# Kernel tuning notes

Hardware: AMD Instinct MI355X
Metric: run time of the kernel (lower is better)

The kernel has to match this reference:

```python
import jax, jax.numpy as jnp
import numpy as np

V, D, G, E, B, S = 50000, 300, 256, 1600000, 64, 64


def setup_inputs() -> dict:
    key = jax.random.key(0)
    k = jax.random.split(key, 6)
    emb = jax.random.normal(k[0], (V, D), jnp.float32) * 0.02
    emb = emb.at[0].set(0.0)  # padding_idx=0
    W1 = jax.random.normal(k[1], (D, G), jnp.float32) * (1.0 / np.sqrt(D))
    b1 = jnp.zeros((G,), jnp.float32)
    W2 = jax.random.normal(k[2], (G, G), jnp.float32) * (1.0 / np.sqrt(G))
    b2 = jnp.zeros((G,), jnp.float32)
    edge_index = jax.random.randint(k[3], (2, E), 0, V, dtype=jnp.int64)
    word_ids = jax.random.randint(k[4], (B, S), 0, V, dtype=jnp.int64)
    return {"emb": emb, "W1": W1, "b1": b1, "W2": W2, "b2": b2,
            "edge_index": edge_index, "word_ids": word_ids}


def _gcn_conv(x, W, b, src, dst, num_nodes):
    """PyG GCNConv: add self-loops, symmetric deg^{-1/2} normalization.
    out_i = sum_{j->i} h_j / sqrt(deg_j * deg_i) + h_i / deg_i + b,
    with deg_i = 1 (self-loop) + in-degree(i), h = x @ W."""
    h = x @ W                                        # (N, G)
    deg = jnp.ones((num_nodes,), h.dtype).at[dst].add(1.0)
    inv_sqrt = jax.lax.rsqrt(deg)                    # (N,)
    coef = inv_sqrt[src] * inv_sqrt[dst]             # (E,)
    agg = jnp.zeros_like(h).at[dst].add(h[src] * coef[:, None])
    agg = agg + h * (inv_sqrt * inv_sqrt)[:, None]   # self-loop term
    return agg + b


def reference(emb, W1, b1, W2, b2, edge_index, word_ids):
    num_nodes = emb.shape[0]
    src, dst = edge_index[0], edge_index[1]
    h = jax.nn.relu(_gcn_conv(emb, W1, b1, src, dst, num_nodes))  # (V, G)
    h = _gcn_conv(h, W2, b2, src, dst, num_nodes)                 # (V, G)
    return h[word_ids]                                            # (B, S, G)
```

## Files before the change

### kernel.cpp

```cpp
#include <hip/hip_runtime.h>
#include <hip/hip_bf16.h>

#define NV 50000
#define ND 300
#define NDP 320
#define NG 256
#define NE 1600000
#define NBS 4096
#define NBUCK 196
#define EPB 8192
#define CPAD 16
#define GEMM1_BLOCKS 782

typedef short short8 __attribute__((ext_vector_type(8)));
typedef float f32x4 __attribute__((ext_vector_type(4)));
typedef float f32x2 __attribute__((ext_vector_type(2)));
typedef _Float16 half4 __attribute__((ext_vector_type(4)));

__device__ __forceinline__ ushort f2bf(float f) {
    unsigned u = __builtin_bit_cast(unsigned, f);
    unsigned r = (u + 0x7fffu + ((u >> 16) & 1u)) >> 16;
    return (ushort)r;
}
__device__ __forceinline__ float bf2f(ushort h) {
    unsigned u = ((unsigned)h) << 16;
    return __builtin_bit_cast(float, u);
}

__global__ __launch_bounds__(256) void hist_bucket(const int* __restrict__ dst,
                                                   int* __restrict__ bucket_count) {
    __shared__ int bh[NBUCK];
    int t = threadIdx.x;
    for (int b = t; b < NBUCK; b += 256) bh[b] = 0;
    __syncthreads();
    for (int i = blockIdx.x * 256 + t; i * 4 < NE; i += gridDim.x * 256) {
        int4 d = *(const int4*)(dst + i * 4);
        atomicAdd(&bh[d.x >> 8], 1);
        atomicAdd(&bh[d.y >> 8], 1);
        atomicAdd(&bh[d.z >> 8], 1);
        atomicAdd(&bh[d.w >> 8], 1);
    }
    __syncthreads();
    for (int b = t; b < NBUCK; b += 256)
        if (bh[b]) atomicAdd(&bucket_count[b * CPAD], bh[b]);
}

__global__ __launch_bounds__(256) void bucket_scan(const int* __restrict__ bucket_count,
                                                   int* __restrict__ bucket_base,
                                                   int* __restrict__ bucket_cursor) {
    __shared__ int s[256];
    int t = threadIdx.x;
    int v = (t < NBUCK) ? bucket_count[t * CPAD] : 0;
    s[t] = v;
    __syncthreads();
    for (int d = 1; d < 256; d <<= 1) {
        int x = (t >= d) ? s[t - d] : 0;
        __syncthreads();
        s[t] += x;
        __syncthreads();
    }
    int excl = s[t] - v;
    if (t < NBUCK) {
        bucket_base[t] = excl;
        bucket_cursor[t * CPAD] = excl;
    }
    if (t == 255) bucket_base[NBUCK] = s[255];
}

__global__ __launch_bounds__(256) void splitw_all(const float* __restrict__ W1,
                                                  const float* __restrict__ W2,
                                                  ushort* __restrict__ W1Th,
                                                  ushort* __restrict__ W1Tl,
                                                  ushort* __restrict__ W2Th,
                                                  ushort* __restrict__ W2Tl) {
    int idx = blockIdx.x * 256 + threadIdx.x;
    if (idx < NG * NDP) {
        int n = idx / NDP, k = idx - n * NDP;
        float v = (k < ND) ? W1[(size_t)k * NG + n] : 0.f;
        ushort h = f2bf(v);
        W1Th[idx] = h;
        W1Tl[idx] = f2bf(v - bf2f(h));
    } else {
        int j = idx - NG * NDP;
        if (j >= NG * NG) return;
        int n = j / NG, k = j - n * NG;
        float v = W2[(size_t)k * NG + n];
        ushort h = f2bf(v);
        W2Th[j] = h;
        W2Tl[j] = f2bf(v - bf2f(h));
    }
}

__global__ __launch_bounds__(256) void gemm1_scatter(const float* __restrict__ A,
                                                     const ushort* __restrict__ BTh,
                                                     const ushort* __restrict__ BTl,
                                                     unsigned char* __restrict__ C8,
                                                     const int* __restrict__ ei,
                                                     int* __restrict__ bucket_cursor,
                                                     unsigned* __restrict__ rec) {
    int t = threadIdx.x;
    if (blockIdx.x < GEMM1_BLOCKS) {
        __shared__ short Ah[128][40];
        __shared__ short Bh[128][40];
        __shared__ short Bl[128][40];
        const int lda = ND, ldb = NDP, M = NV, K = ND, KP = NDP;
        int bid = blockIdx.x;
        int bm = (bid % 391) * 128;
        int bn = (bid / 391) * 128;
        int lane = t & 63, wv = t >> 6;
        int wm = (wv >> 1) * 64, wn = (wv & 1) * 64;
        int srow = t >> 1;
        int skq = (t & 1) * 16;
        f32x4 acc[4][4];
#pragma unroll
        for (int mi = 0; mi < 4; ++mi)
#pragma unroll
            for (int ni = 0; ni < 4; ++ni) acc[mi][ni] = (f32x4)0.0f;

        for (int k0 = 0; k0 < KP; k0 += 32) {
            int gk = k0 + skq;
            {
                int gr = bm + srow;
                short va[16];
                float v[16];
                if (gr < M && gk < K) {
                    if (gk + 16 <= K) {
#pragma unroll
                        for (int q = 0; q < 4; ++q) {
                            float4 p = *(const float4*)(A + (size_t)gr * lda + gk + q * 4);
                            v[q * 4 + 0] = p.x; v[q * 4 + 1] = p.y;
                            v[q * 4 + 2] = p.z; v[q * 4 + 3] = p.w;
                        }
                    } else {
#pragma unroll
                        for (int e = 0; e < 16; ++e)
                            v[e] = (gk + e < K) ? A[(size_t)gr * lda + gk + e] : 0.f;
                    }
                } else {
#pragma unroll
                    for (int e = 0; e < 16; ++e) v[e] = 0.f;
                }
#pragma unroll
                for (int e = 0; e < 16; ++e) va[e] = (short)f2bf(v[e]);
                *(short8*)&Ah[srow][skq] = *(short8*)&va[0];
                *(short8*)&Ah[srow][skq + 8] = *(short8*)&va[8];
            }
            {
                int nr = bn + srow;
                short8 bh0 = *(const short8*)(BTh + (size_t)nr * ldb + gk);
                short8 bh1 = *(const short8*)(BTh + (size_t)nr * ldb + gk + 8);
                short8 bl0 = *(const short8*)(BTl + (size_t)nr * ldb + gk);
                short8 bl1 = *(const short8*)(BTl + (size_t)nr * ldb + gk + 8);
                *(short8*)&Bh[srow][skq] = bh0;
                *(short8*)&Bh[srow][skq + 8] = bh1;
                *(short8*)&Bl[srow][skq] = bl0;
                *(short8*)&Bl[srow][skq + 8] = bl1;
            }
            __syncthreads();
            int m16 = lane & 15, kb = (lane >> 4) * 8;
            short8 a_h[4], b_h[4], b_l[4];
#pragma unroll
            for (int mi = 0; mi < 4; ++mi)
                a_h[mi] = *(const short8*)&Ah[wm + mi * 16 + m16][kb];
#pragma unroll
            for (int ni = 0; ni < 4; ++ni) {
                b_h[ni] = *(const short8*)&Bh[wn + ni * 16 + m16][kb];
                b_l[ni] = *(const short8*)&Bl[wn + ni * 16 + m16][kb];
            }
#pragma unroll
            for (int mi = 0; mi < 4; ++mi)
#pragma unroll
                for (int ni = 0; ni < 4; ++ni) {
                    acc[mi][ni] = __builtin_amdgcn_mfma_f32_16x16x32_bf16(a_h[mi], b_h[ni], acc[mi][ni], 0, 0, 0);
                    acc[mi][ni] = __builtin_amdgcn_mfma_f32_16x16x32_bf16(a_h[mi], b_l[ni], acc[mi][ni], 0, 0, 0);
                }
            __syncthreads();
        }
        int m16 = lane & 15, rq = lane >> 4;
#pragma unroll
        for (int mi = 0; mi < 4; ++mi)
#pragma unroll
            for (int ni = 0; ni < 4; ++ni) {
                int row0 = bm + wm + mi * 16 + rq * 4;
                int col = bn + wn + ni * 16 + m16;
                int p01 = __builtin_amdgcn_cvt_pk_fp8_f32(acc[mi][ni][0], acc[mi][ni][1], 0, false);
                int p23 = __builtin_amdgcn_cvt_pk_fp8_f32(acc[mi][ni][2], acc[mi][ni][3], 0, false);
                if (row0 + 0 < M) C8[(size_t)(row0 + 0) * NG + col] = (unsigned char)(p01 & 0xff);
                if (row0 + 1 < M) C8[(size_t)(row0 + 1) * NG + col] = (unsigned char)((p01 >> 8) & 0xff);
                if (row0 + 2 < M) C8[(size_t)(row0 + 2) * NG + col] = (unsigned char)(p23 & 0xff);
                if (row0 + 3 < M) C8[(size_t)(row0 + 3) * NG + col] = (unsigned char)((p23 >> 8) & 0xff);
            }
    } else {
        __shared__ int cnt[NBUCK];
        __shared__ int basel[NBUCK];
        int e0 = (blockIdx.x - GEMM1_BLOCKS) * EPB;
        for (int b = t; b < NBUCK; b += 256) cnt[b] = 0;
        __syncthreads();
        for (int q = 0; q < EPB / 1024; ++q) {
            int i4 = e0 + q * 1024 + t * 4;
            if (i4 < NE) {
                int4 d = *(const int4*)(ei + NE + i4);
                atomicAdd(&cnt[d.x >> 8], 1);
                atomicAdd(&cnt[d.y >> 8], 1);
                atomicAdd(&cnt[d.z >> 8], 1);
                atomicAdd(&cnt[d.w >> 8], 1);
            }
        }
        __syncthreads();
        for (int b = t; b < NBUCK; b += 256) {
            int c = cnt[b];
            basel[b] = c ? atomicAdd(&bucket_cursor[b * CPAD], c) : 0;
        }
        __syncthreads();
        for (int b = t; b < NBUCK; b += 256) cnt[b] = 0;
        __syncthreads();
        for (int q = 0; q < EPB / 1024; ++q) {
            int i4 = e0 + q * 1024 + t * 4;
            if (i4 < NE) {
                int4 s = *(const int4*)(ei + i4);
                int4 d = *(const int4*)(ei + NE + i4);
                int b0 = d.x >> 8, b1 = d.y >> 8, b2 = d.z >> 8, b3 = d.w >> 8;
                int r0 = atomicAdd(&cnt[b0], 1);
                rec[basel[b0] + r0] = (unsigned)s.x | ((unsigned)(d.x & 255) << 16);
                int r1 = atomicAdd(&cnt[b1], 1);
                rec[basel[b1] + r1] = (unsigned)s.y | ((unsigned)(d.y & 255) << 16);
                int r2 = atomicAdd(&cnt[b2], 1);
                rec[basel[b2] + r2] = (unsigned)s.z | ((unsigned)(d.z & 255) << 16);
                int r3 = atomicAdd(&cnt[b3], 1);
                rec[basel[b3] + r3] = (unsigned)s.w | ((unsigned)(d.w & 255) << 16);
            }
        }
    }
}

__global__ __launch_bounds__(256) void csr_build(const unsigned* __restrict__ rec,
                                                 const int* __restrict__ bucket_base,
                                                 int* __restrict__ off,
                                                 float* __restrict__ inv_sqrt,
                                                 ushort* __restrict__ csr_src) {
    __shared__ int degl[256];
    __shared__ int s[256];
    int b = blockIdx.x, t = threadIdx.x;
    degl[t] = 0;
    __syncthreads();
    int r0 = bucket_base[b], r1 = bucket_base[b + 1];
    for (int i = r0 + t; i < r1; i += 256)
        atomicAdd(&degl[(rec[i] >> 16) & 255], 1);
    __syncthreads();
    int v = degl[t];
    s[t] = v;
    __syncthreads();
    for (int d = 1; d < 256; d <<= 1) {
        int x = (t >= d) ? s[t - d] : 0;
        __syncthreads();
        s[t] += x;
        __syncthreads();
    }
    int excl = s[t] - v + r0;
    int n = (b << 8) + t;
    if (n < NV) {
        off[n] = excl;
        inv_sqrt[n] = rsqrtf((float)(v + 1));
    }
    if (b == NBUCK - 1 && t == 0) off[NV] = NE;
    __syncthreads();
    degl[t] = excl;
    __syncthreads();
    for (int i = r0 + t; i < r1; i += 256) {
        unsigned e = rec[i];
        int p = atomicAdd(&degl[(e >> 16) & 255], 1);
        csr_src[p] = (ushort)(e & 0xffff);
    }
}

__global__ __launch_bounds__(256) void gemm_out(const float* __restrict__ A,
                                                int lda,
                                                const ushort* __restrict__ BTh,
                                                const ushort* __restrict__ BTl,
                                                int ldb,
                                                int M, int K, int KP,
                                                float* __restrict__ C32,
                                                const float* __restrict__ bias) {
    __shared__ short Ah[128][40];
    __shared__ short Bh[128][40];
    __shared__ short Bl[128][40];
    int t = threadIdx.x;
    int bm = blockIdx.x * 128;
    int bn = blockIdx.y * 128;
    int lane = t & 63, wv = t >> 6;
    int wm = (wv >> 1) * 64, wn = (wv & 1) * 64;
    int srow = t >> 1;
    int skq = (t & 1) * 16;
    f32x4 acc[4][4];
#pragma unroll
    for (int mi = 0; mi < 4; ++mi)
#pragma unroll
        for (int ni = 0; ni < 4; ++ni) acc[mi][ni] = (f32x4)0.0f;

    for (int k0 = 0; k0 < KP; k0 += 32) {
        int gk = k0 + skq;
        {
            int gr = bm + srow;
            short va[16];
            float v[16];
            if (gr < M && gk < K) {
#pragma unroll
                for (int q = 0; q < 4; ++q) {
                    float4 p = *(const float4*)(A + (size_t)gr * lda + gk + q * 4);
                    v[q * 4 + 0] = p.x; v[q * 4 + 1] = p.y;
                    v[q * 4 + 2] = p.z; v[q * 4 + 3] = p.w;
                }
            } else {
#pragma unroll
                for (int e = 0; e < 16; ++e) v[e] = 0.f;
            }
#pragma unroll
            for (int e = 0; e < 16; ++e) va[e] = (short)f2bf(v[e]);
            *(short8*)&Ah[srow][skq] = *(short8*)&va[0];
            *(short8*)&Ah[srow][skq + 8] = *(short8*)&va[8];
        }
        {
            int nr = bn + srow;
            short8 bh0 = *(const short8*)(BTh + (size_t)nr * ldb + gk);
            short8 bh1 = *(const short8*)(BTh + (size_t)nr * ldb + gk + 8);
            short8 bl0 = *(const short8*)(BTl + (size_t)nr * ldb + gk);
            short8 bl1 = *(const short8*)(BTl + (size_t)nr * ldb + gk + 8);
            *(short8*)&Bh[srow][skq] = bh0;
            *(short8*)&Bh[srow][skq + 8] = bh1;
            *(short8*)&Bl[srow][skq] = bl0;
            *(short8*)&Bl[srow][skq + 8] = bl1;
        }
        __syncthreads();
        int m16 = lane & 15, kb = (lane >> 4) * 8;
        short8 a_h[4], b_h[4], b_l[4];
#pragma unroll
        for (int mi = 0; mi < 4; ++mi)
            a_h[mi] = *(const short8*)&Ah[wm + mi * 16 + m16][kb];
#pragma unroll
        for (int ni = 0; ni < 4; ++ni) {
            b_h[ni] = *(const short8*)&Bh[wn + ni * 16 + m16][kb];
            b_l[ni] = *(const short8*)&Bl[wn + ni * 16 + m16][kb];
        }
#pragma unroll
        for (int mi = 0; mi < 4; ++mi)
#pragma unroll
            for (int ni = 0; ni < 4; ++ni) {
                acc[mi][ni] = __builtin_amdgcn_mfma_f32_16x16x32_bf16(a_h[mi], b_h[ni], acc[mi][ni], 0, 0, 0);
                acc[mi][ni] = __builtin_amdgcn_mfma_f32_16x16x32_bf16(a_h[mi], b_l[ni], acc[mi][ni], 0, 0, 0);
            }
        __syncthreads();
    }
    int m16 = lane & 15, rq = lane >> 4;
#pragma unroll
    for (int mi = 0; mi < 4; ++mi)
#pragma unroll
        for (int ni = 0; ni < 4; ++ni) {
#pragma unroll
            for (int r = 0; r < 4; ++r) {
                int row = bm + wm + mi * 16 + rq * 4 + r;
                int col = bn + wn + ni * 16 + m16;
                if (row < M)
                    C32[(size_t)row * NG + col] = acc[mi][ni][r] + bias[col];
            }
        }
}

__global__ __launch_bounds__(256) void agg1_kernel(const unsigned char* __restrict__ h1f8,
                                                   const int* __restrict__ off,
                                                   const ushort* __restrict__ csr_src,
                                                   const float* __restrict__ inv_sqrt,
                                                   const float* __restrict__ b1,
                                                   _Float16* __restrict__ x1) {
    int wv = threadIdx.x >> 6, lane = threadIdx.x & 63;
    int i = blockIdx.x * 4 + wv;
    if (i >= NV) return;
    int c4 = lane * 4;
    int s0 = off[i], s1 = off[i + 1];
    float a0 = 0.f, a1 = 0.f, a2 = 0.f, a3 = 0.f;
    int j = s0;
    for (; j + 16 <= s1; j += 16) {
        int sx[16];
        float wx[16];
        unsigned pk[16];
#pragma unroll
        for (int u = 0; u < 16; ++u) sx[u] = csr_src[j + u];
#pragma unroll
        for (int u = 0; u < 16; ++u) {
            wx[u] = inv_sqrt[sx[u]];
            pk[u] = *(const unsigned*)(h1f8 + (size_t)sx[u] * NG + c4);
        }
#pragma unroll
        for (int u = 0; u < 16; ++u) {
            f32x2 v01 = __builtin_amdgcn_cvt_pk_f32_fp8(pk[u], false);
            f32x2 v23 = __builtin_amdgcn_cvt_pk_f32_fp8(pk[u], true);
            a0 += wx[u] * v01[0];
            a1 += wx[u] * v01[1];
            a2 += wx[u] * v23[0];
            a3 += wx[u] * v23[1];
        }
    }
    for (; j + 4 <= s1; j += 4) {
        int sx[4];
        float wx[4];
        unsigned pk[4];
#pragma unroll
        for (int u = 0; u < 4; ++u) sx[u] = csr_src[j + u];
#pragma unroll
        for (int u = 0; u < 4; ++u) {
            wx[u] = inv_sqrt[sx[u]];
            pk[u] = *(const unsigned*)(h1f8 + (size_t)sx[u] * NG + c4);
        }
#pragma unroll
        for (int u = 0; u < 4; ++u) {
            f32x2 v01 = __builtin_amdgcn_cvt_pk_f32_fp8(pk[u], false);
            f32x2 v23 = __builtin_amdgcn_cvt_pk_f32_fp8(pk[u], true);
            a0 += wx[u] * v01[0];
            a1 += wx[u] * v01[1];
            a2 += wx[u] * v23[0];
            a3 += wx[u] * v23[1];
        }
    }
    for (; j < s1; ++j) {
        int s = csr_src[j];
        float w = inv_sqrt[s];
        unsigned pk = *(const unsigned*)(h1f8 + (size_t)s * NG + c4);
        f32x2 v01 = __builtin_amdgcn_cvt_pk_f32_fp8(pk, false);
        f32x2 v23 = __builtin_amdgcn_cvt_pk_f32_fp8(pk, true);
        a0 += w * v01[0];
        a1 += w * v01[1];
        a2 += w * v23[0];
        a3 += w * v23[1];
    }
    float is = inv_sqrt[i], is2 = is * is;
    unsigned pks = *(const unsigned*)(h1f8 + (size_t)i * NG + c4);
    f32x2 s01 = __builtin_amdgcn_cvt_pk_f32_fp8(pks, false);
    f32x2 s23 = __builtin_amdgcn_cvt_pk_f32_fp8(pks, true);
    float4 bb = *(const float4*)(b1 + c4);
    half4 o;
    o[0] = (_Float16)fmaxf(is * a0 + s01[0] * is2 + bb.x, 0.f);
    o[1] = (_Float16)fmaxf(is * a1 + s01[1] * is2 + bb.y, 0.f);
    o[2] = (_Float16)fmaxf(is * a2 + s23[0] * is2 + bb.z, 0.f);
    o[3] = (_Float16)fmaxf(is * a3 + s23[1] * is2 + bb.w, 0.f);
    *(half4*)(x1 + (size_t)i * NG + c4) = o;
}

__global__ __launch_bounds__(256) void agg2_kernel(const _Float16* __restrict__ x1,
                                                   const int* __restrict__ off,
                                                   const ushort* __restrict__ csr_src,
                                                   const float* __restrict__ inv_sqrt,
                                                   const int* __restrict__ word_ids,
                                                   float* __restrict__ y) {
    int wv = threadIdx.x >> 6, lane = threadIdx.x & 63;
    int p = blockIdx.x * 4 + wv;
    if (p >= NBS) return;
    int n = word_ids[p];
    int c4 = lane * 4;
    int s0 = off[n], s1 = off[n + 1];
    float a0 = 0.f, a1 = 0.f, a2 = 0.f, a3 = 0.f;
    int j = s0;
    for (; j + 16 <= s1; j += 16) {
        int sx[16];
        float wx[16];
        half4 vx[16];
#pragma unroll
        for (int u = 0; u < 16; ++u) sx[u] = csr_src[j + u];
#pragma unroll
        for (int u = 0; u < 16; ++u) {
            wx[u] = inv_sqrt[sx[u]];
            vx[u] = *(const half4*)(x1 + (size_t)sx[u] * NG + c4);
        }
#pragma unroll
        for (int u = 0; u < 16; ++u) {
            a0 += wx[u] * (float)vx[u][0];
            a1 += wx[u] * (float)vx[u][1];
            a2 += wx[u] * (float)vx[u][2];
            a3 += wx[u] * (float)vx[u][3];
        }
    }
    for (; j + 4 <= s1; j += 4) {
        int sx[4];
        float wx[4];
        half4 vx[4];
#pragma unroll
        for (int u = 0; u < 4; ++u) sx[u] = csr_src[j + u];
#pragma unroll
        for (int u = 0; u < 4; ++u) {
            wx[u] = inv_sqrt[sx[u]];
            vx[u] = *(const half4*)(x1 + (size_t)sx[u] * NG + c4);
        }
#pragma unroll
        for (int u = 0; u < 4; ++u) {
            a0 += wx[u] * (float)vx[u][0];
            a1 += wx[u] * (float)vx[u][1];
            a2 += wx[u] * (float)vx[u][2];
            a3 += wx[u] * (float)vx[u][3];
        }
    }
    for (; j < s1; ++j) {
        int s = csr_src[j];
        float w = inv_sqrt[s];
        half4 hv = *(const half4*)(x1 + (size_t)s * NG + c4);
        a0 += w * (float)hv[0];
        a1 += w * (float)hv[1];
        a2 += w * (float)hv[2];
        a3 += w * (float)hv[3];
    }
    float is = inv_sqrt[n], is2 = is * is;
    half4 sv = *(const half4*)(x1 + (size_t)n * NG + c4);
    float4 o;
    o.x = is * a0 + (float)sv[0] * is2;
    o.y = is * a1 + (float)sv[1] * is2;
    o.z = is * a2 + (float)sv[2] * is2;
    o.w = is * a3 + (float)sv[3] * is2;
    *(float4*)(y + (size_t)p * NG + c4) = o;
}

extern "C" void kernel_launch(void* const* d_in, const int* in_sizes, int n_in,
                              void* d_out, int out_size, void* d_ws, size_t ws_size,
                              hipStream_t stream) {
    const float* emb = (const float*)d_in[0];
    const float* W1  = (const float*)d_in[1];
    const float* b1  = (const float*)d_in[2];
    const float* W2  = (const float*)d_in[3];
    const float* b2  = (const float*)d_in[4];
    const int*   ei  = (const int*)d_in[5];
    const int*   wid = (const int*)d_in[6];
    float* out = (float*)d_out;

    char* w = (char*)d_ws;
    auto alloc = [&](size_t bytes) {
        void* p = (void*)w;
        w += (bytes + 255) & ~(size_t)255;
        return p;
    };
    int*    off      = (int*)alloc((size_t)(NV + 1) * 4);
    float*  inv_sqrt = (float*)alloc((size_t)NV * 4);
    int*    bucket_count  = (int*)alloc((size_t)NBUCK * CPAD * 4);
    int*    bucket_base   = (int*)alloc((size_t)(NBUCK + 1) * 4);
    int*    bucket_cursor = (int*)alloc((size_t)NBUCK * CPAD * 4);
    ushort* csr_src  = (ushort*)alloc((size_t)NE * 2);
    unsigned* bucket_rec = (unsigned*)alloc((size_t)NE * 4);
    ushort* W1T_h    = (ushort*)alloc((size_t)NG * NDP * 2);
    ushort* W1T_l    = (ushort*)alloc((size_t)NG * NDP * 2);
    ushort* W2T_h    = (ushort*)alloc((size_t)NG * NG * 2);
    ushort* W2T_l    = (ushort*)alloc((size_t)NG * NG * 2);
    unsigned char* h1f8 = (unsigned char*)alloc((size_t)NV * NG);
    _Float16* x1     = (_Float16*)alloc((size_t)NV * NG * 2);
    float*  y        = (float*)alloc((size_t)NBS * NG * 4);

    hipMemsetAsync(bucket_count, 0, (size_t)NBUCK * CPAD * 4, stream);

    splitw_all<<<(NG * NDP + NG * NG + 255) / 256, 256, 0, stream>>>(W1, W2, W1T_h, W1T_l,
                                                                     W2T_h, W2T_l);
    hist_bucket<<<1024, 256, 0, stream>>>(ei + NE, bucket_count);
    bucket_scan<<<1, 256, 0, stream>>>(bucket_count, bucket_base, bucket_cursor);
    gemm1_scatter<<<GEMM1_BLOCKS + NBUCK, 256, 0, stream>>>(emb, W1T_h, W1T_l, h1f8,
                                                            ei, bucket_cursor, bucket_rec);
    csr_build<<<NBUCK, 256, 0, stream>>>(bucket_rec, bucket_base, off, inv_sqrt, csr_src);

    agg1_kernel<<<(NV + 3) / 4, 256, 0, stream>>>(h1f8, off, csr_src, inv_sqrt, b1, x1);
    agg2_kernel<<<(NBS + 3) / 4, 256, 0, stream>>>(x1, off, csr_src, inv_sqrt, wid, y);
    {
        dim3 grid((NBS + 127) / 128, NG / 128);
        gemm_out<<<grid, 256, 0, stream>>>(y, NG, W2T_h, W2T_l, NG,
                                           NBS, NG, NG, out, b2);
    }
}
```

Baseline: 197.0 us.

## Merge weight split with edge histogram; drop low-bf16 correction in first GEMM

Fuses the weight transpose/split kernel and the destination histogram kernel into one launch, removing a kernel boundary. The first GEMM no longer loads or multiplies the low-order bf16 part of W1, halving its MFMA work and shared-memory traffic. Its block index mapping also changes so that the two N-tiles sharing an M-tile run in adjacent blocks, which improves reuse of the A rows in cache. Dropping the W1 correction term lowers GEMM1 precision, though the output is already quantised to fp8.

```diff
diff --git a/kernel.cpp b/kernel.cpp
--- a/kernel.cpp
+++ b/kernel.cpp
@@ -11,6 +11,9 @@
 #define EPB 8192
 #define CPAD 16
 #define GEMM1_BLOCKS 782
+#define PREP_W1 320
+#define PREP_W2 256
+#define PREP_HIST 1024
 
 typedef short short8 __attribute__((ext_vector_type(8)));
 typedef float f32x4 __attribute__((ext_vector_type(4)));
@@ -27,22 +30,45 @@
     return __builtin_bit_cast(float, u);
 }
 
-__global__ __launch_bounds__(256) void hist_bucket(const int* __restrict__ dst,
+__global__ __launch_bounds__(256) void prep_kernel(const float* __restrict__ W1,
+                                                   const float* __restrict__ W2,
+                                                   ushort* __restrict__ W1Th,
+                                                   ushort* __restrict__ W1Tl,
+                                                   ushort* __restrict__ W2Th,
+                                                   ushort* __restrict__ W2Tl,
+                                                   const int* __restrict__ dst,
                                                    int* __restrict__ bucket_count) {
-    __shared__ int bh[NBUCK];
     int t = threadIdx.x;
-    for (int b = t; b < NBUCK; b += 256) bh[b] = 0;
-    __syncthreads();
-    for (int i = blockIdx.x * 256 + t; i * 4 < NE; i += gridDim.x * 256) {
-        int4 d = *(const int4*)(dst + i * 4);
-        atomicAdd(&bh[d.x >> 8], 1);
-        atomicAdd(&bh[d.y >> 8], 1);
-        atomicAdd(&bh[d.z >> 8], 1);
-        atomicAdd(&bh[d.w >> 8], 1);
-    }
-    __syncthreads();
-    for (int b = t; b < NBUCK; b += 256)
-        if (bh[b]) atomicAdd(&bucket_count[b * CPAD], bh[b]);
+    if (blockIdx.x < PREP_W1) {
+        int idx = blockIdx.x * 256 + t;
+        int n = idx / NDP, k = idx - n * NDP;
+        float v = (k < ND) ? W1[(size_t)k * NG + n] : 0.f;
+        ushort h = f2bf(v);
+        W1Th[idx] = h;
+        W1Tl[idx] = f2bf(v - bf2f(h));
+    } else if (blockIdx.x < PREP_W1 + PREP_W2) {
+        int j = (blockIdx.x - PREP_W1) * 256 + t;
+        int n = j / NG, k = j - n * NG;
+        float v = W2[(size_t)k * NG + n];
+        ushort h = f2bf(v);
+        W2Th[j] = h;
+        W2Tl[j] = f2bf(v - bf2f(h));
+    } else {
+        __shared__ int bh[NBUCK];
+        for (int b = t; b < NBUCK; b += 256) bh[b] = 0;
+        __syncthreads();
+        int blk = blockIdx.x - (PREP_W1 + PREP_W2);
+        for (int i = blk * 256 + t; i * 4 < NE; i += PREP_HIST * 256) {
+            int4 d = *(const int4*)(dst + i * 4);
+            atomicAdd(&bh[d.x >> 8], 1);
+            atomicAdd(&bh[d.y >> 8], 1);
+            atomicAdd(&bh[d.z >> 8], 1);
+            atomicAdd(&bh[d.w >> 8], 1);
+        }
+        __syncthreads();
+        for (int b = t; b < NBUCK; b += 256)
+            if (bh[b]) atomicAdd(&bucket_count[b * CPAD], bh[b]);
+    }
 }
 
 __global__ __launch_bounds__(256) void bucket_scan(const int* __restrict__ bucket_count,
@@ -67,33 +93,8 @@
     if (t == 255) bucket_base[NBUCK] = s[255];
 }
 
-__global__ __launch_bounds__(256) void splitw_all(const float* __restrict__ W1,
-                                                  const float* __restrict__ W2,
-                                                  ushort* __restrict__ W1Th,
-                                                  ushort* __restrict__ W1Tl,
-                                                  ushort* __restrict__ W2Th,
-                                                  ushort* __restrict__ W2Tl) {
-    int idx = blockIdx.x * 256 + threadIdx.x;
-    if (idx < NG * NDP) {
-        int n = idx / NDP, k = idx - n * NDP;
-        float v = (k < ND) ? W1[(size_t)k * NG + n] : 0.f;
-        ushort h = f2bf(v);
-        W1Th[idx] = h;
-        W1Tl[idx] = f2bf(v - bf2f(h));
-    } else {
-        int j = idx - NG * NDP;
-        if (j >= NG * NG) return;
-        int n = j / NG, k = j - n * NG;
-        float v = W2[(size_t)k * NG + n];
-        ushort h = f2bf(v);
-        W2Th[j] = h;
-        W2Tl[j] = f2bf(v - bf2f(h));
-    }
-}
-
 __global__ __launch_bounds__(256) void gemm1_scatter(const float* __restrict__ A,
                                                      const ushort* __restrict__ BTh,
-                                                     const ushort* __restrict__ BTl,
                                                      unsigned char* __restrict__ C8,
                                                      const int* __restrict__ ei,
                                                      int* __restrict__ bucket_cursor,
@@ -102,11 +103,10 @@
     if (blockIdx.x < GEMM1_BLOCKS) {
         __shared__ short Ah[128][40];
         __shared__ short Bh[128][40];
-        __shared__ short Bl[128][40];
         const int lda = ND, ldb = NDP, M = NV, K = ND, KP = NDP;
         int bid = blockIdx.x;
-        int bm = (bid % 391) * 128;
-        int bn = (bid / 391) * 128;
+        int bm = (bid >> 1) * 128;
+        int bn = (bid & 1) * 128;
         int lane = t & 63, wv = t >> 6;
         int wm = (wv >> 1) * 64, wn = (wv & 1) * 64;
         int srow = t >> 1;
@@ -149,31 +149,23 @@
                 int nr = bn + srow;
                 short8 bh0 = *(const short8*)(BTh + (size_t)nr * ldb + gk);
                 short8 bh1 = *(const short8*)(BTh + (size_t)nr * ldb + gk + 8);
-                short8 bl0 = *(const short8*)(BTl + (size_t)nr * ldb + gk);
-                short8 bl1 = *(const short8*)(BTl + (size_t)nr * ldb + gk + 8);
                 *(short8*)&Bh[srow][skq] = bh0;
                 *(short8*)&Bh[srow][skq + 8] = bh1;
-                *(short8*)&Bl[srow][skq] = bl0;
-                *(short8*)&Bl[srow][skq + 8] = bl1;
             }
             __syncthreads();
             int m16 = lane & 15, kb = (lane >> 4) * 8;
-            short8 a_h[4], b_h[4], b_l[4];
+            short8 a_h[4], b_h[4];
 #pragma unroll
             for (int mi = 0; mi < 4; ++mi)
                 a_h[mi] = *(const short8*)&Ah[wm + mi * 16 + m16][kb];
 #pragma unroll
-            for (int ni = 0; ni < 4; ++ni) {
+            for (int ni = 0; ni < 4; ++ni)
                 b_h[ni] = *(const short8*)&Bh[wn + ni * 16 + m16][kb];
-                b_l[ni] = *(const short8*)&Bl[wn + ni * 16 + m16][kb];
-            }
 #pragma unroll
             for (int mi = 0; mi < 4; ++mi)
 #pragma unroll
-                for (int ni = 0; ni < 4; ++ni) {
+                for (int ni = 0; ni < 4; ++ni)
                     acc[mi][ni] = __builtin_amdgcn_mfma_f32_16x16x32_bf16(a_h[mi], b_h[ni], acc[mi][ni], 0, 0, 0);
-                    acc[mi][ni] = __builtin_amdgcn_mfma_f32_16x16x32_bf16(a_h[mi], b_l[ni], acc[mi][ni], 0, 0, 0);
-                }
             __syncthreads();
         }
         int m16 = lane & 15, rq = lane >> 4;
@@ -550,11 +542,10 @@
 
     hipMemsetAsync(bucket_count, 0, (size_t)NBUCK * CPAD * 4, stream);
 
-    splitw_all<<<(NG * NDP + NG * NG + 255) / 256, 256, 0, stream>>>(W1, W2, W1T_h, W1T_l,
-                                                                     W2T_h, W2T_l);
-    hist_bucket<<<1024, 256, 0, stream>>>(ei + NE, bucket_count);
+    prep_kernel<<<PREP_W1 + PREP_W2 + PREP_HIST, 256, 0, stream>>>(
+        W1, W2, W1T_h, W1T_l, W2T_h, W2T_l, ei + NE, bucket_count);
     bucket_scan<<<1, 256, 0, stream>>>(bucket_count, bucket_base, bucket_cursor);
-    gemm1_scatter<<<GEMM1_BLOCKS + NBUCK, 256, 0, stream>>>(emb, W1T_h, W1T_l, h1f8,
+    gemm1_scatter<<<GEMM1_BLOCKS + NBUCK, 256, 0, stream>>>(emb, W1T_h, h1f8,
                                                             ei, bucket_cursor, bucket_rec);
     csr_build<<<NBUCK, 256, 0, stream>>>(bucket_rec, bucket_base, off, inv_sqrt, csr_src);
 
```

Result: faster. 191.5 us (-2.8%).
